# Performance work log

Hardware: AMD Instinct MI355X
Metric: run time of the kernel (lower is better)

The kernel has to match this reference:

```python
import jax, jax.numpy as jnp
import numpy as np

B, T, D, H = 4, 2048, 1024, 16
DH = D // H          # 64
HALF = DH // 2       # 32


def _rope_tables(T, half, base=10000.0):
    inv_freq = 1.0 / (base ** (np.arange(half, dtype=np.float32) / half))
    t = np.arange(T, dtype=np.float32)
    ang = np.outer(t, inv_freq)                       # [T, half]
    cos = jnp.asarray(np.cos(ang))[None, None]        # [1,1,T,half]
    sin = jnp.asarray(np.sin(ang))[None, None]
    return cos, sin


def setup_inputs() -> dict:
    key = jax.random.key(0)
    kx, kq, kp = jax.random.split(key, 3)
    cos, sin = _rope_tables(T, HALF)
    return {
        "x": jax.random.normal(kx, (B, T, D), dtype=jnp.float32),
        "cos": cos,
        "sin": sin,
        "W_qkv": jax.random.normal(kq, (3 * D, D), dtype=jnp.float32) * (D ** -0.5),
        "W_proj": jax.random.normal(kp, (D, D), dtype=jnp.float32) * (D ** -0.5),
    }


def _apply_rope(q, k, cos, sin):
    # q,k: [B,H,T,dh]; cos,sin: [1,1,T,dh/2]
    t = q.shape[2]
    c, s = cos[:, :, :t, :], sin[:, :, :t, :]
    h = q.shape[-1] // 2
    q1, q2 = q[..., :h], q[..., h:]
    k1, k2 = k[..., :h], k[..., h:]
    q_rot = jnp.concatenate([q1 * c - q2 * s, q1 * s + q2 * c], axis=-1)
    k_rot = jnp.concatenate([k1 * c - k2 * s, k1 * s + k2 * c], axis=-1)
    return q_rot, k_rot


def reference(x, cos, sin, W_qkv, W_proj):
    Bb, Tt, C = x.shape
    qkv = x @ W_qkv.T                                 # [B,T,3C]
    q, k, v = jnp.split(qkv, 3, axis=2)
    # [B,T,C] -> [B,H,T,dh]
    q = q.reshape(Bb, Tt, H, DH).transpose(0, 2, 1, 3)
    k = k.reshape(Bb, Tt, H, DH).transpose(0, 2, 1, 3)
    v = v.reshape(Bb, Tt, H, DH).transpose(0, 2, 1, 3)
    q, k = _apply_rope(q, k, cos, sin)
    w = jnp.einsum("bhqd,bhkd->bhqk", q, k) * (DH ** -0.5)
    causal = jnp.tril(jnp.ones((Tt, Tt), dtype=bool))
    w = jnp.where(causal, w, -jnp.inf)
    w = jax.nn.softmax(w.astype(jnp.float32), axis=-1).astype(x.dtype)
    out = jnp.einsum("bhqk,bhkd->bhqd", w, v)
    # XSA: subtract self-value contribution (diagonal attention weight)
    self_w = jnp.diagonal(w, axis1=-2, axis2=-1)[..., None]  # [B,H,T,1]
    out = out - self_w * v
    out = out.transpose(0, 2, 1, 3).reshape(Bb, Tt, C)
    return out @ W_proj.T
```

## Files before the change

### kernel.cpp

```cpp
#include <hip/hip_runtime.h>

constexpr int Tq = 2048;
constexpr int Dq = 1024;

typedef __bf16 bf16x8 __attribute__((ext_vector_type(8)));
typedef float f32x4 __attribute__((ext_vector_type(4)));
typedef _Float16 f16;
typedef f16 f16x4 __attribute__((ext_vector_type(4)));
typedef unsigned short u16;
typedef u16 u16x4 __attribute__((ext_vector_type(4)));
typedef u16 u16x8 __attribute__((ext_vector_type(8)));

__device__ __forceinline__ u16 f2bf(float f) {
    unsigned int u = __float_as_uint(f);
    u += 0x7fffu + ((u >> 16) & 1u);
    return (u16)(u >> 16);
}

__device__ __forceinline__ void gld_lds16(const void* g, void* l) {
    __builtin_amdgcn_global_load_lds(
        (const __attribute__((address_space(1))) unsigned int*)g,
        (__attribute__((address_space(3))) unsigned int*)l, 16, 0, 0);
}

__global__ void cvt3_f32_bf16(const float* __restrict__ a, u16* __restrict__ oa, int na,
                              const float* __restrict__ b, u16* __restrict__ ob, int nb,
                              const float* __restrict__ c, u16* __restrict__ oc, int nc) {
    int i = blockIdx.x * 256 + threadIdx.x;
    const float* in; u16* out;
    if (i < na) { in = a; out = oa; }
    else if (i < na + nb) { in = b; out = ob; i -= na; }
    else if (i < na + nb + nc) { in = c; out = oc; i -= na + nb; }
    else return;
    float4 v = ((const float4*)in)[i];
    u16x4 o;
    o.x = f2bf(v.x); o.y = f2bf(v.y); o.z = f2bf(v.z); o.w = f2bf(v.w);
    ((u16x4*)out)[i] = o;
}

__global__ __launch_bounds__(256) void gemm_qkv(const u16* __restrict__ A,
                                                const u16* __restrict__ B,
                                                const float* __restrict__ cosT,
                                                const float* __restrict__ sinT,
                                                u16* __restrict__ Qb,
                                                u16* __restrict__ Kb,
                                                f16* __restrict__ Vtg) {
    constexpr int K = 1024, N = 3072;
    __shared__ u16 As[128 * 32];
    __shared__ u16 Bs[128 * 32];
    const int t = threadIdx.x;
    const int lane = t & 63;
    const int wave = t >> 6;
    const int l16 = lane & 15;
    const int quad = lane >> 4;
    const int bm = blockIdx.x * 128;
    const int by = blockIdx.y;
    const int bn = by * 128;
    const int wm = (wave & 1) * 64;
    const int wn = (wave >> 1) * 64;
    const int srow = t >> 2;
    const int scol = (t & 3) * 8;

    f32x4 acc[4][4] = {};

    const u16* Ab = A + (size_t)(bm + srow) * K + scol;
    const u16* Bb = B + (size_t)(bn + srow) * K + scol;

    for (int k0 = 0; k0 < K; k0 += 32) {
        gld_lds16(Ab + k0,                    (char*)As + t * 16);
        gld_lds16(Ab + (size_t)64 * K + k0,   (char*)As + 4096 + t * 16);
        gld_lds16(Bb + k0,                    (char*)Bs + t * 16);
        gld_lds16(Bb + (size_t)64 * K + k0,   (char*)Bs + 4096 + t * 16);
        __syncthreads();

        bf16x8 af[4], bf[4];
#pragma unroll
        for (int i = 0; i < 4; i++) {
            af[i] = *(const bf16x8*)&As[(wm + i * 16 + l16) * 32 + quad * 8];
            bf[i] = *(const bf16x8*)&Bs[(wn + i * 16 + l16) * 32 + quad * 8];
        }
#pragma unroll
        for (int i = 0; i < 4; i++)
#pragma unroll
            for (int j = 0; j < 4; j++)
                acc[i][j] = __builtin_amdgcn_mfma_f32_16x16x32_bf16(af[i], bf[j], acc[i][j], 0, 0, 0);
        __syncthreads();
    }

    const int kind = by >> 3;
    if (kind < 2) {
        u16* Out = kind ? Kb : Qb;
        const float qscale = kind ? 1.f : 0.18033688011112042f;
        const int h = ((by & 7) << 1) + (wn >> 6);
#pragma unroll
        for (int i = 0; i < 4; i++)
#pragma unroll
            for (int r = 0; r < 4; r++) {
                const int gm = bm + wm + i * 16 + quad * 4 + r;
                const int b = gm >> 11, tt = gm & 2047;
                const size_t row = ((size_t)(b * 16 + h) * Tq + tt) * 64;
#pragma unroll
                for (int jj = 0; jj < 2; jj++) {
                    const int dd = jj * 16 + l16;
                    const float c = cosT[tt * 32 + dd];
                    const float s = sinT[tt * 32 + dd];
                    const float v1 = acc[i][jj][r];
                    const float v2 = acc[i][jj + 2][r];
                    Out[row + dd]      = f2bf((v1 * c - v2 * s) * qscale);
                    Out[row + dd + 32] = f2bf((v1 * s + v2 * c) * qscale);
                }
            }
    } else {
#pragma unroll
        for (int i = 0; i < 4; i++) {
            const int gm0 = bm + wm + i * 16 + quad * 4;
            const int b = gm0 >> 11, tt = gm0 & 2047;
#pragma unroll
            for (int j = 0; j < 4; j++) {
                const int col = wn + j * 16 + l16;
                const int h = ((by & 7) << 1) + (col >> 6);
                const int d = col & 63;
                f16x4 o = {(f16)acc[i][j][0], (f16)acc[i][j][1],
                           (f16)acc[i][j][2], (f16)acc[i][j][3]};
                *(f16x4*)&Vtg[((size_t)(b * 16 + h) * 64 + d) * Tq + tt] = o;
            }
        }
    }
}

__global__ __launch_bounds__(256) void gemm_bt(const u16* __restrict__ A,
                                               const u16* __restrict__ B,
                                               float* __restrict__ Cv,
                                               int M, int N, int K) {
    __shared__ u16 As[128 * 32];
    __shared__ u16 Bs[128 * 32];
    const int t = threadIdx.x;
    const int lane = t & 63;
    const int wave = t >> 6;
    const int l16 = lane & 15;
    const int quad = lane >> 4;
    const int bm = blockIdx.x * 128;
    const int bn = blockIdx.y * 128;
    const int wm = (wave & 1) * 64;
    const int wn = (wave >> 1) * 64;
    const int srow = t >> 2;
    const int scol = (t & 3) * 8;

    f32x4 acc[4][4] = {};

    const u16* Ab = A + (size_t)(bm + srow) * K + scol;
    const u16* Bb = B + (size_t)(bn + srow) * K + scol;

    for (int k0 = 0; k0 < K; k0 += 32) {
        gld_lds16(Ab + k0,                    (char*)As + t * 16);
        gld_lds16(Ab + (size_t)64 * K + k0,   (char*)As + 4096 + t * 16);
        gld_lds16(Bb + k0,                    (char*)Bs + t * 16);
        gld_lds16(Bb + (size_t)64 * K + k0,   (char*)Bs + 4096 + t * 16);
        __syncthreads();

        bf16x8 af[4], bf[4];
#pragma unroll
        for (int i = 0; i < 4; i++) {
            af[i] = *(const bf16x8*)&As[(wm + i * 16 + l16) * 32 + quad * 8];
            bf[i] = *(const bf16x8*)&Bs[(wn + i * 16 + l16) * 32 + quad * 8];
        }
#pragma unroll
        for (int i = 0; i < 4; i++)
#pragma unroll
            for (int j = 0; j < 4; j++)
                acc[i][j] = __builtin_amdgcn_mfma_f32_16x16x32_bf16(af[i], bf[j], acc[i][j], 0, 0, 0);
        __syncthreads();
    }

#pragma unroll
    for (int i = 0; i < 4; i++)
#pragma unroll
        for (int j = 0; j < 4; j++)
#pragma unroll
            for (int r = 0; r < 4; r++) {
                const int gm = bm + wm + i * 16 + quad * 4 + r;
                const int gn = bn + wn + j * 16 + l16;
                Cv[(size_t)gm * N + gn] = acc[i][j][r];
            }
}

template <bool MASK>
__device__ __forceinline__ void flash_tile(const u16* __restrict__ Ks,
                                           const f16* __restrict__ Vs,
                                           const bf16x8& qf0, const bf16x8& qf1,
                                           int l16, int quad, int i_loc,
                                           float& l_run, f32x4* o_acc) {
    f32x4 s[4];
    const int cp0 = quad ^ (l16 & 7);
    const int cp1 = (4 + quad) ^ (l16 & 7);
    __builtin_amdgcn_s_setprio(1);
#pragma unroll
    for (int tn = 0; tn < 4; tn++) {
        const int jrow = tn * 16 + l16;
        bf16x8 kf0 = *(const bf16x8*)&Ks[jrow * 64 + cp0 * 8];
        bf16x8 kf1 = *(const bf16x8*)&Ks[jrow * 64 + cp1 * 8];
        f32x4 z = {0.f, 0.f, 0.f, 0.f};
        z = __builtin_amdgcn_mfma_f32_16x16x32_bf16(kf0, qf0, z, 0, 0, 0);
        z = __builtin_amdgcn_mfma_f32_16x16x32_bf16(kf1, qf1, z, 0, 0, 0);
        s[tn] = z;
    }
    __builtin_amdgcn_s_setprio(0);
    float rsa[4];
#pragma unroll
    for (int tn = 0; tn < 4; tn++) {
        float rs = 0.f;
#pragma unroll
        for (int r = 0; r < 4; r++) {
            float v = s[tn][r];
            if (MASK) {
                const int j_loc = tn * 16 + quad * 4 + r;
                if (j_loc > i_loc) v = -1e30f;
            }
            float p = exp2f(v);
            rs += p;
            if (MASK) {
                const int j_loc = tn * 16 + quad * 4 + r;
                if (j_loc == i_loc) p = 0.f;
            }
            s[tn][r] = p;
        }
        rsa[tn] = rs;
    }
    l_run += (rsa[0] + rsa[1]) + (rsa[2] + rsa[3]);

    f16x4 pf[4];
#pragma unroll
    for (int tk = 0; tk < 4; tk++)
        pf[tk] = f16x4{(f16)s[tk][0], (f16)s[tk][1], (f16)s[tk][2], (f16)s[tk][3]};
    __builtin_amdgcn_s_setprio(1);
#pragma unroll
    for (int td = 0; td < 4; td++) {
        const int drow = td * 16 + l16;
#pragma unroll
        for (int tk = 0; tk < 4; tk++) {
            const int cp = (2 * tk + (quad >> 1)) ^ (l16 & 7);
            f16x4 vf = *(const f16x4*)&Vs[drow * 64 + cp * 8 + (quad & 1) * 4];
            o_acc[td] = __builtin_amdgcn_mfma_f32_16x16x16f16(vf, pf[tk], o_acc[td], 0, 0, 0);
        }
    }
    __builtin_amdgcn_s_setprio(0);
}

__global__ __launch_bounds__(256, 2) void flash(const u16* __restrict__ Qb,
                                                const u16* __restrict__ Kb,
                                                const f16* __restrict__ Vtg,
                                                u16* __restrict__ Ob) {
    __shared__ __align__(16) char smem[65536];

    const int t = threadIdx.x, lane = t & 63, wave = t >> 6;
    const int l16 = lane & 15, quad = lane >> 4;
    const int i = blockIdx.x;
    const int xcd = i & 7, w = i >> 3;
    const int bh = xcd * 8 + (w >> 4);
    const int b = bh >> 4, h = bh & 15;
    const int x = w & 15;
    const int qtA = x, qtB = 31 - x;
    const int q0a = qtA * 64, q0b = qtB * 64;
    const u16* Qp = Qb + (size_t)bh * Tq * 64;
    const u16* Kp = Kb + (size_t)bh * Tq * 64;
    const f16* Vp = Vtg + (size_t)bh * 64 * Tq;

    const int rowi = wave * 16 + l16;
    bf16x8 qa0 = *(const bf16x8*)(Qp + (size_t)(q0a + rowi) * 64 + quad * 8);
    bf16x8 qa1 = *(const bf16x8*)(Qp + (size_t)(q0a + rowi) * 64 + 32 + quad * 8);
    bf16x8 qb0 = *(const bf16x8*)(Qp + (size_t)(q0b + rowi) * 64 + quad * 8);
    bf16x8 qb1 = *(const bf16x8*)(Qp + (size_t)(q0b + rowi) * 64 + 32 + quad * 8);
    asm volatile("s_waitcnt vmcnt(0)"
                 : "+v"(qa0), "+v"(qa1), "+v"(qb0), "+v"(qb1) :: "memory");

    float lA = 0.f, lB = 0.f;
    f32x4 oA[4] = {}, oB[4] = {};

    const int sr = t >> 3;
    const int sc = (t & 7) ^ (sr & 7);
    const int i_tloc = wave * 16 + l16;
    const int nt = 32 - x;
    const int nt2 = (nt + 1) >> 1;

    auto stage = [&](int n2) {
        const int j0 = n2 * 128;
        char* buf = smem + (n2 & 1) * 32768;
        gld_lds16(Kp + (size_t)(j0 + sr) * 64 + sc * 8,            buf + t * 16);
        gld_lds16(Kp + (size_t)(j0 + 32 + sr) * 64 + sc * 8,       buf + 4096 + t * 16);
        gld_lds16(Kp + (size_t)(j0 + 64 + sr) * 64 + sc * 8,       buf + 8192 + t * 16);
        gld_lds16(Kp + (size_t)(j0 + 96 + sr) * 64 + sc * 8,       buf + 12288 + t * 16);
        gld_lds16(Vp + (size_t)sr * Tq + j0 + sc * 8,              buf + 16384 + t * 16);
        gld_lds16(Vp + (size_t)(32 + sr) * Tq + j0 + sc * 8,       buf + 20480 + t * 16);
        gld_lds16(Vp + (size_t)sr * Tq + j0 + 64 + sc * 8,         buf + 24576 + t * 16);
        gld_lds16(Vp + (size_t)(32 + sr) * Tq + j0 + 64 + sc * 8,  buf + 28672 + t * 16);
    };

    stage(0);
    for (int n2 = 0; n2 < nt2; n2++) {
        asm volatile("s_waitcnt vmcnt(0)\n\ts_barrier" ::: "memory");
        if (n2 + 1 < nt2) stage(n2 + 1);
        char* cb = smem + (n2 & 1) * 32768;
#pragma unroll
        for (int s = 0; s < 2; s++) {
            const int tile = n2 * 2 + s;
            const u16* Ks = (const u16*)(cb + s * 8192);
            const f16* Vs = (const f16*)(cb + 16384 + s * 8192);
            if (tile < qtB)
                flash_tile<false>(Ks, Vs, qb0, qb1, l16, quad, i_tloc, lB, oB);
            else if (tile == qtB)
                flash_tile<true>(Ks, Vs, qb0, qb1, l16, quad, i_tloc, lB, oB);
            if (tile < qtA)
                flash_tile<false>(Ks, Vs, qa0, qa1, l16, quad, i_tloc, lA, oA);
            else if (tile == qtA)
                flash_tile<true>(Ks, Vs, qa0, qa1, l16, quad, i_tloc, lA, oA);
        }
    }

    lA += __shfl_xor(lA, 16, 64);
    lA += __shfl_xor(lA, 32, 64);
    lB += __shfl_xor(lB, 16, 64);
    lB += __shfl_xor(lB, 32, 64);
    const float ivA = 1.f / lA, ivB = 1.f / lB;

    __syncthreads();
    u16* Os = (u16*)smem;
#pragma unroll
    for (int td = 0; td < 4; td++) {
        u16x4 oa, ob;
#pragma unroll
        for (int r = 0; r < 4; r++) {
            oa[r] = f2bf(oA[td][r] * ivA);
            ob[r] = f2bf(oB[td][r] * ivB);
        }
        *(u16x4*)&Os[wave * 1152 + l16 * 72 + td * 16 + quad * 4] = oa;
        *(u16x4*)&Os[(4 + wave) * 1152 + l16 * 72 + td * 16 + quad * 4] = ob;
    }
    __syncthreads();
    const int oi = lane >> 2, od = (lane & 3) * 16;
    {
        u16x8 r0 = *(const u16x8*)&Os[wave * 1152 + oi * 72 + od];
        u16x8 r1 = *(const u16x8*)&Os[wave * 1152 + oi * 72 + od + 8];
        const size_t orow = ((size_t)b * Tq + q0a + wave * 16 + oi) * Dq + h * 64 + od;
        *(u16x8*)&Ob[orow] = r0;
        *(u16x8*)&Ob[orow + 8] = r1;
    }
    {
        u16x8 r0 = *(const u16x8*)&Os[(4 + wave) * 1152 + oi * 72 + od];
        u16x8 r1 = *(const u16x8*)&Os[(4 + wave) * 1152 + oi * 72 + od + 8];
        const size_t orow = ((size_t)b * Tq + q0b + wave * 16 + oi) * Dq + h * 64 + od;
        *(u16x8*)&Ob[orow] = r0;
        *(u16x8*)&Ob[orow + 8] = r1;
    }
}

extern "C" void kernel_launch(void* const* d_in, const int* in_sizes, int n_in,
                              void* d_out, int out_size, void* d_ws, size_t ws_size,
                              hipStream_t stream) {
    const float* x     = (const float*)d_in[0];
    const float* cosT  = (const float*)d_in[1];
    const float* sinT  = (const float*)d_in[2];
    const float* Wqkv  = (const float*)d_in[3];
    const float* Wproj = (const float*)d_in[4];

    u16* xb     = (u16*)d_ws;
    u16* wqkvb  = xb + (size_t)8192 * 1024;
    u16* wprojb = wqkvb + (size_t)3072 * 1024;
    u16* Qb     = wprojb + (size_t)1024 * 1024;
    u16* Kb     = Qb + (size_t)64 * 2048 * 64;
    f16* Vtg    = (f16*)(Kb + (size_t)64 * 2048 * 64);
    u16* attn   = (u16*)(Vtg + (size_t)64 * 64 * 2048);

    cvt3_f32_bf16<<<12288, 256, 0, stream>>>(x, xb, 2097152,
                                             Wqkv, wqkvb, 786432,
                                             Wproj, wprojb, 262144);

    gemm_qkv<<<dim3(64, 24), 256, 0, stream>>>(xb, wqkvb, cosT, sinT, Qb, Kb, Vtg);
    flash<<<1024, 256, 0, stream>>>(Qb, Kb, Vtg, attn);
    gemm_bt<<<dim3(64, 8), 256, 0, stream>>>(attn, wprojb, (float*)d_out, 8192, 1024, 1024);
}
```

Measured before the change: 269.7 us.

## Process four query tiles per flash block to reuse each K/V tile

Each flash attention block now owns four query tiles (x, x+8, 23-x, 31-x) instead of two, and the grid shrinks from 1024 to 512 blocks. Every K/V tile staged in shared memory is now consumed by up to four Q tiles. Masked diagonal tiles and fully skipped tiles are handled per tile with runtime predicates. This halves global K/V traffic and staging per unit of work, and the causal workload stays balanced across blocks. The cost is much higher register pressure from four sets of accumulators and scores, plus more branching, which could cause spills or cut occupancy.

```diff
diff --git a/kernel.cpp b/kernel.cpp
--- a/kernel.cpp
+++ b/kernel.cpp
@@ -184,13 +184,42 @@
             }
 }
 
-template <bool MASK>
-__device__ __forceinline__ void flash_tile(const u16* __restrict__ Ks,
-                                           const f16* __restrict__ Vs,
-                                           const bf16x8& qf0, const bf16x8& qf1,
-                                           int l16, int quad, int i_loc,
-                                           float& l_run, f32x4* o_acc) {
-    f32x4 s[4];
+#define SMAX(S, LR, DIAG)                                                     \
+    do {                                                                      \
+        float ra_ = 0.f;                                                      \
+        if (DIAG) {                                                           \
+            _Pragma("unroll") for (int tn_ = 0; tn_ < 4; tn_++)               \
+                _Pragma("unroll") for (int r_ = 0; r_ < 4; r_++) {            \
+                    const int jl_ = tn_ * 16 + quad * 4 + r_;                 \
+                    float v_ = S[tn_][r_];                                    \
+                    if (jl_ > i_loc) v_ = -1e30f;                             \
+                    float p_ = exp2f(v_);                                     \
+                    ra_ += p_;                                                \
+                    if (jl_ == i_loc) p_ = 0.f;                               \
+                    S[tn_][r_] = p_;                                          \
+                }                                                             \
+        } else {                                                              \
+            _Pragma("unroll") for (int tn_ = 0; tn_ < 4; tn_++)               \
+                _Pragma("unroll") for (int r_ = 0; r_ < 4; r_++) {            \
+                    float p_ = exp2f(S[tn_][r_]);                             \
+                    ra_ += p_;                                                \
+                    S[tn_][r_] = p_;                                          \
+                }                                                             \
+        }                                                                     \
+        LR += ra_;                                                            \
+    } while (0)
+
+__device__ __forceinline__ void flash_tile4(
+    const u16* __restrict__ Ks, const f16* __restrict__ Vs, int tile,
+    int qt0, int qt1, int qt2, int qt3,
+    const bf16x8& q00, const bf16x8& q01, const bf16x8& q10, const bf16x8& q11,
+    const bf16x8& q20, const bf16x8& q21, const bf16x8& q30, const bf16x8& q31,
+    int l16, int quad, int i_loc,
+    float& l0, f32x4* o0, float& l1, f32x4* o1,
+    float& l2, f32x4* o2, float& l3, f32x4* o3) {
+    const bool a0 = tile <= qt0, a1 = tile <= qt1, a2 = tile <= qt2;
+    const bool d0 = tile == qt0, d1 = tile == qt1, d2 = tile == qt2, d3 = tile == qt3;
+    f32x4 s0[4], s1[4], s2[4], s3[4];
     const int cp0 = quad ^ (l16 & 7);
     const int cp1 = (4 + quad) ^ (l16 & 7);
     __builtin_amdgcn_s_setprio(1);
@@ -200,38 +229,54 @@
         bf16x8 kf0 = *(const bf16x8*)&Ks[jrow * 64 + cp0 * 8];
         bf16x8 kf1 = *(const bf16x8*)&Ks[jrow * 64 + cp1 * 8];
         f32x4 z = {0.f, 0.f, 0.f, 0.f};
-        z = __builtin_amdgcn_mfma_f32_16x16x32_bf16(kf0, qf0, z, 0, 0, 0);
-        z = __builtin_amdgcn_mfma_f32_16x16x32_bf16(kf1, qf1, z, 0, 0, 0);
-        s[tn] = z;
+        z = __builtin_amdgcn_mfma_f32_16x16x32_bf16(kf0, q30, z, 0, 0, 0);
+        z = __builtin_amdgcn_mfma_f32_16x16x32_bf16(kf1, q31, z, 0, 0, 0);
+        s3[tn] = z;
+        if (a2) {
+            f32x4 z2 = {0.f, 0.f, 0.f, 0.f};
+            z2 = __builtin_amdgcn_mfma_f32_16x16x32_bf16(kf0, q20, z2, 0, 0, 0);
+            z2 = __builtin_amdgcn_mfma_f32_16x16x32_bf16(kf1, q21, z2, 0, 0, 0);
+            s2[tn] = z2;
+        }
+        if (a1) {
+            f32x4 z1 = {0.f, 0.f, 0.f, 0.f};
+            z1 = __builtin_amdgcn_mfma_f32_16x16x32_bf16(kf0, q10, z1, 0, 0, 0);
+            z1 = __builtin_amdgcn_mfma_f32_16x16x32_bf16(kf1, q11, z1, 0, 0, 0);
+            s1[tn] = z1;
+        }
+        if (a0) {
+            f32x4 z0 = {0.f, 0.f, 0.f, 0.f};
+            z0 = __builtin_amdgcn_mfma_f32_16x16x32_bf16(kf0, q00, z0, 0, 0, 0);
+            z0 = __builtin_amdgcn_mfma_f32_16x16x32_bf16(kf1, q01, z0, 0, 0, 0);
+            s0[tn] = z0;
+        }
     }
     __builtin_amdgcn_s_setprio(0);
-    float rsa[4];
-#pragma unroll
-    for (int tn = 0; tn < 4; tn++) {
-        float rs = 0.f;
-#pragma unroll
-        for (int r = 0; r < 4; r++) {
-            float v = s[tn][r];
-            if (MASK) {
-                const int j_loc = tn * 16 + quad * 4 + r;
-                if (j_loc > i_loc) v = -1e30f;
-            }
-            float p = exp2f(v);
-            rs += p;
-            if (MASK) {
-                const int j_loc = tn * 16 + quad * 4 + r;
-                if (j_loc == i_loc) p = 0.f;
-            }
-            s[tn][r] = p;
-        }
-        rsa[tn] = rs;
-    }
-    l_run += (rsa[0] + rsa[1]) + (rsa[2] + rsa[3]);
-
-    f16x4 pf[4];
+
+    SMAX(s3, l3, d3);
+    if (a2) SMAX(s2, l2, d2);
+    if (a1) SMAX(s1, l1, d1);
+    if (a0) SMAX(s0, l0, d0);
+
+    f16x4 pf0[4], pf1[4], pf2[4], pf3[4];
 #pragma unroll
     for (int tk = 0; tk < 4; tk++)
-        pf[tk] = f16x4{(f16)s[tk][0], (f16)s[tk][1], (f16)s[tk][2], (f16)s[tk][3]};
+        pf3[tk] = f16x4{(f16)s3[tk][0], (f16)s3[tk][1], (f16)s3[tk][2], (f16)s3[tk][3]};
+    if (a2) {
+#pragma unroll
+        for (int tk = 0; tk < 4; tk++)
+            pf2[tk] = f16x4{(f16)s2[tk][0], (f16)s2[tk][1], (f16)s2[tk][2], (f16)s2[tk][3]};
+    }
+    if (a1) {
+#pragma unroll
+        for (int tk = 0; tk < 4; tk++)
+            pf1[tk] = f16x4{(f16)s1[tk][0], (f16)s1[tk][1], (f16)s1[tk][2], (f16)s1[tk][3]};
+    }
+    if (a0) {
+#pragma unroll
+        for (int tk = 0; tk < 4; tk++)
+            pf0[tk] = f16x4{(f16)s0[tk][0], (f16)s0[tk][1], (f16)s0[tk][2], (f16)s0[tk][3]};
+    }
     __builtin_amdgcn_s_setprio(1);
 #pragma unroll
     for (int td = 0; td < 4; td++) {
@@ -240,7 +285,10 @@
         for (int tk = 0; tk < 4; tk++) {
             const int cp = (2 * tk + (quad >> 1)) ^ (l16 & 7);
             f16x4 vf = *(const f16x4*)&Vs[drow * 64 + cp * 8 + (quad & 1) * 4];
-            o_acc[td] = __builtin_amdgcn_mfma_f32_16x16x16f16(vf, pf[tk], o_acc[td], 0, 0, 0);
+            o3[td] = __builtin_amdgcn_mfma_f32_16x16x16f16(vf, pf3[tk], o3[td], 0, 0, 0);
+            if (a2) o2[td] = __builtin_amdgcn_mfma_f32_16x16x16f16(vf, pf2[tk], o2[td], 0, 0, 0);
+            if (a1) o1[td] = __builtin_amdgcn_mfma_f32_16x16x16f16(vf, pf1[tk], o1[td], 0, 0, 0);
+            if (a0) o0[td] = __builtin_amdgcn_mfma_f32_16x16x16f16(vf, pf0[tk], o0[td], 0, 0, 0);
         }
     }
     __builtin_amdgcn_s_setprio(0);
@@ -256,25 +304,29 @@
     const int l16 = lane & 15, quad = lane >> 4;
     const int i = blockIdx.x;
     const int xcd = i & 7, w = i >> 3;
-    const int bh = xcd * 8 + (w >> 4);
+    const int bh = xcd * 8 + (w >> 3);
     const int b = bh >> 4, h = bh & 15;
-    const int x = w & 15;
-    const int qtA = x, qtB = 31 - x;
-    const int q0a = qtA * 64, q0b = qtB * 64;
+    const int x = w & 7;
+    const int qt0 = x, qt1 = x + 8, qt2 = 23 - x, qt3 = 31 - x;
     const u16* Qp = Qb + (size_t)bh * Tq * 64;
     const u16* Kp = Kb + (size_t)bh * Tq * 64;
     const f16* Vp = Vtg + (size_t)bh * 64 * Tq;
 
     const int rowi = wave * 16 + l16;
-    bf16x8 qa0 = *(const bf16x8*)(Qp + (size_t)(q0a + rowi) * 64 + quad * 8);
-    bf16x8 qa1 = *(const bf16x8*)(Qp + (size_t)(q0a + rowi) * 64 + 32 + quad * 8);
-    bf16x8 qb0 = *(const bf16x8*)(Qp + (size_t)(q0b + rowi) * 64 + quad * 8);
-    bf16x8 qb1 = *(const bf16x8*)(Qp + (size_t)(q0b + rowi) * 64 + 32 + quad * 8);
+    bf16x8 q00 = *(const bf16x8*)(Qp + (size_t)(qt0 * 64 + rowi) * 64 + quad * 8);
+    bf16x8 q01 = *(const bf16x8*)(Qp + (size_t)(qt0 * 64 + rowi) * 64 + 32 + quad * 8);
+    bf16x8 q10 = *(const bf16x8*)(Qp + (size_t)(qt1 * 64 + rowi) * 64 + quad * 8);
+    bf16x8 q11 = *(const bf16x8*)(Qp + (size_t)(qt1 * 64 + rowi) * 64 + 32 + quad * 8);
+    bf16x8 q20 = *(const bf16x8*)(Qp + (size_t)(qt2 * 64 + rowi) * 64 + quad * 8);
+    bf16x8 q21 = *(const bf16x8*)(Qp + (size_t)(qt2 * 64 + rowi) * 64 + 32 + quad * 8);
+    bf16x8 q30 = *(const bf16x8*)(Qp + (size_t)(qt3 * 64 + rowi) * 64 + quad * 8);
+    bf16x8 q31 = *(const bf16x8*)(Qp + (size_t)(qt3 * 64 + rowi) * 64 + 32 + quad * 8);
     asm volatile("s_waitcnt vmcnt(0)"
-                 : "+v"(qa0), "+v"(qa1), "+v"(qb0), "+v"(qb1) :: "memory");
-
-    float lA = 0.f, lB = 0.f;
-    f32x4 oA[4] = {}, oB[4] = {};
+                 : "+v"(q00), "+v"(q01), "+v"(q10), "+v"(q11),
+                   "+v"(q20), "+v"(q21), "+v"(q30), "+v"(q31) :: "memory");
+
+    float l0 = 0.f, l1 = 0.f, l2 = 0.f, l3 = 0.f;
+    f32x4 o0[4] = {}, o1[4] = {}, o2[4] = {}, o3[4] = {};
 
     const int sr = t >> 3;
     const int sc = (t & 7) ^ (sr & 7);
@@ -303,51 +355,48 @@
 #pragma unroll
         for (int s = 0; s < 2; s++) {
             const int tile = n2 * 2 + s;
-            const u16* Ks = (const u16*)(cb + s * 8192);
-            const f16* Vs = (const f16*)(cb + 16384 + s * 8192);
-            if (tile < qtB)
-                flash_tile<false>(Ks, Vs, qb0, qb1, l16, quad, i_tloc, lB, oB);
-            else if (tile == qtB)
-                flash_tile<true>(Ks, Vs, qb0, qb1, l16, quad, i_tloc, lB, oB);
-            if (tile < qtA)
-                flash_tile<false>(Ks, Vs, qa0, qa1, l16, quad, i_tloc, lA, oA);
-            else if (tile == qtA)
-                flash_tile<true>(Ks, Vs, qa0, qa1, l16, quad, i_tloc, lA, oA);
-        }
-    }
-
-    lA += __shfl_xor(lA, 16, 64);
-    lA += __shfl_xor(lA, 32, 64);
-    lB += __shfl_xor(lB, 16, 64);
-    lB += __shfl_xor(lB, 32, 64);
-    const float ivA = 1.f / lA, ivB = 1.f / lB;
+            if (tile <= qt3) {
+                const u16* Ks = (const u16*)(cb + s * 8192);
+                const f16* Vs = (const f16*)(cb + 16384 + s * 8192);
+                flash_tile4(Ks, Vs, tile, qt0, qt1, qt2, qt3,
+                            q00, q01, q10, q11, q20, q21, q30, q31,
+                            l16, quad, i_tloc, l0, o0, l1, o1, l2, o2, l3, o3);
+            }
+        }
+    }
+
+    l0 += __shfl_xor(l0, 16, 64); l0 += __shfl_xor(l0, 32, 64);
+    l1 += __shfl_xor(l1, 16, 64); l1 += __shfl_xor(l1, 32, 64);
+    l2 += __shfl_xor(l2, 16, 64); l2 += __shfl_xor(l2, 32, 64);
+    l3 += __shfl_xor(l3, 16, 64); l3 += __shfl_xor(l3, 32, 64);
+    const float iv0 = 1.f / l0, iv1 = 1.f / l1, iv2 = 1.f / l2, iv3 = 1.f / l3;
 
     __syncthreads();
     u16* Os = (u16*)smem;
 #pragma unroll
     for (int td = 0; td < 4; td++) {
-        u16x4 oa, ob;
+        u16x4 w0, w1, w2, w3;
 #pragma unroll
         for (int r = 0; r < 4; r++) {
-            oa[r] = f2bf(oA[td][r] * ivA);
-            ob[r] = f2bf(oB[td][r] * ivB);
-        }
-        *(u16x4*)&Os[wave * 1152 + l16 * 72 + td * 16 + quad * 4] = oa;
-        *(u16x4*)&Os[(4 + wave) * 1152 + l16 * 72 + td * 16 + quad * 4] = ob;
+            w0[r] = f2bf(o0[td][r] * iv0);
+            w1[r] = f2bf(o1[td][r] * iv1);
+            w2[r] = f2bf(o2[td][r] * iv2);
+            w3[r] = f2bf(o3[td][r] * iv3);
+        }
+        const int base = l16 * 72 + td * 16 + quad * 4;
+        *(u16x4*)&Os[(0 * 4 + wave) * 1152 + base] = w0;
+        *(u16x4*)&Os[(1 * 4 + wave) * 1152 + base] = w1;
+        *(u16x4*)&Os[(2 * 4 + wave) * 1152 + base] = w2;
+        *(u16x4*)&Os[(3 * 4 + wave) * 1152 + base] = w3;
     }
     __syncthreads();
     const int oi = lane >> 2, od = (lane & 3) * 16;
-    {
-        u16x8 r0 = *(const u16x8*)&Os[wave * 1152 + oi * 72 + od];
-        u16x8 r1 = *(const u16x8*)&Os[wave * 1152 + oi * 72 + od + 8];
-        const size_t orow = ((size_t)b * Tq + q0a + wave * 16 + oi) * Dq + h * 64 + od;
-        *(u16x8*)&Ob[orow] = r0;
-        *(u16x8*)&Ob[orow + 8] = r1;
-    }
-    {
-        u16x8 r0 = *(const u16x8*)&Os[(4 + wave) * 1152 + oi * 72 + od];
-        u16x8 r1 = *(const u16x8*)&Os[(4 + wave) * 1152 + oi * 72 + od + 8];
-        const size_t orow = ((size_t)b * Tq + q0b + wave * 16 + oi) * Dq + h * 64 + od;
+#pragma unroll
+    for (int s = 0; s < 4; s++) {
+        const int qts = (s == 0) ? qt0 : (s == 1) ? qt1 : (s == 2) ? qt2 : qt3;
+        u16x8 r0 = *(const u16x8*)&Os[(s * 4 + wave) * 1152 + oi * 72 + od];
+        u16x8 r1 = *(const u16x8*)&Os[(s * 4 + wave) * 1152 + oi * 72 + od + 8];
+        const size_t orow = ((size_t)b * Tq + qts * 64 + wave * 16 + oi) * Dq + h * 64 + od;
         *(u16x8*)&Ob[orow] = r0;
         *(u16x8*)&Ob[orow + 8] = r1;
     }
@@ -375,6 +424,6 @@
                                              Wproj, wprojb, 262144);
 
     gemm_qkv<<<dim3(64, 24), 256, 0, stream>>>(xb, wqkvb, cosT, sinT, Qb, Kb, Vtg);
-    flash<<<1024, 256, 0, stream>>>(Qb, Kb, Vtg, attn);
+    flash<<<512, 256, 0, stream>>>(Qb, Kb, Vtg, attn);
     gemm_bt<<<dim3(64, 8), 256, 0, stream>>>(attn, wprojb, (float*)d_out, 8192, 1024, 1024);
 }
```

Result: slower. 981.9 us (+264.0%).
